# Performance work log

Measured on AMD Instinct MI355X. Metric: run time of the kernel, lower is better.

Reference implementation:

```python
import jax, jax.numpy as jnp
import numpy as np

B, T, I, U, S = 1024, 256, 64, 1024, 64  # batch, warmup_len, num_input_signals, units, output_steps


def setup_inputs() -> dict:
    key = jax.random.key(0)
    ks = jax.random.split(key, 4)
    s = lambda n: 1.0 / np.sqrt(n)
    inputs = jax.random.normal(ks[0], (B, T, I), jnp.float32)
    Wk = jax.random.normal(ks[1], (I, 4 * U), jnp.float32) * s(I)   # input kernel (gate order i,f,g,o)
    Wr = jax.random.normal(ks[2], (U, 4 * U), jnp.float32) * s(U)   # recurrent kernel
    b = jnp.zeros((4 * U,), jnp.float32)
    Wd = jax.random.normal(ks[3], (U, I), jnp.float32) * s(U)       # dense head
    bd = jnp.zeros((I,), jnp.float32)
    output_indices = jnp.arange(2, dtype=jnp.int32)
    return {"inputs": inputs, "Wk": Wk, "Wr": Wr, "b": b, "Wd": Wd, "bd": bd,
            "output_indices": output_indices, "output_steps": S}


def _lstm_step(h, c, x, Wk, Wr, b):
    # Keras LSTMCell math, gate order i, f, g(candidate), o
    z = x @ Wk + h @ Wr + b
    i, f, g, o = jnp.split(z, 4, axis=-1)
    c = jax.nn.sigmoid(f) * c + jax.nn.sigmoid(i) * jnp.tanh(g)
    h = jax.nn.sigmoid(o) * jnp.tanh(c)
    return h, c


def reference(inputs, Wk, Wr, b, Wd, bd, output_indices, output_steps):
    Bn = inputs.shape[0]
    Un = Wr.shape[0]
    h0 = jnp.zeros((Bn, Un), inputs.dtype)
    c0 = jnp.zeros((Bn, Un), inputs.dtype)

    # warmup: run LSTM over the input sequence, keep final state only
    def warm(carry, x_t):
        h, c = carry
        h, c = _lstm_step(h, c, x_t, Wk, Wr, b)
        return (h, c), None

    (h, c), _ = jax.lax.scan(warm, (h0, c0), jnp.swapaxes(inputs, 0, 1))
    pred = h @ Wd + bd  # first prediction [B, I]

    def dec(carry, _):
        h, c, p = carry
        h, c = _lstm_step(h, c, p, Wk, Wr, b)
        p = h @ Wd + bd
        return (h, c, p), p

    _, rest = jax.lax.scan(dec, (h, c, pred), None, length=output_steps - 1)
    preds = jnp.concatenate([pred[None], rest], axis=0)   # [S, B, I]
    preds = jnp.swapaxes(preds, 0, 1)                     # [B, S, I]
    return jnp.take(preds, output_indices, axis=-1)       # [B, S, len(output_indices)]
```

## Files before the change

### kernel.cpp

```cpp
#include <hip/hip_runtime.h>
#include <hip/hip_bf16.h>
#include <stdint.h>


typedef _Float16 f16;
typedef _Float16 f16x8 __attribute__((ext_vector_type(8)));
typedef float f32x4 __attribute__((ext_vector_type(4)));

#define TILE_HALVES 8192
#define NKZ 17
#define NKH 16

__device__ __forceinline__ int swz(int r, int k) { return (r * 64 + k) ^ ((r & 7) << 3); }

__device__ __forceinline__ void stage8k(const f16* __restrict__ g, f16* l, int tid) {
  const int wave = tid >> 6, lane = tid & 63;
  const char* gp = (const char*)g;
  char* lp = (char*)l;
#pragma unroll
  for (int i = 0; i < 4; i++) {
    const int off = i * 4096 + wave * 1024;
    __builtin_amdgcn_global_load_lds(
        (const __attribute__((address_space(1))) unsigned int*)(gp + off + lane * 16),
        (__attribute__((address_space(3))) unsigned int*)(lp + off), 16, 0, 0);
  }
}
__device__ __forceinline__ void stage4k(const f16* __restrict__ g, f16* l, int tid) {
  const int wave = tid >> 6, lane = tid & 63;
  const char* gp = (const char*)g;
  char* lp = (char*)l;
#pragma unroll
  for (int i = 0; i < 2; i++) {
    const int off = i * 4096 + wave * 1024;
    __builtin_amdgcn_global_load_lds(
        (const __attribute__((address_space(1))) unsigned int*)(gp + off + lane * 16),
        (__attribute__((address_space(3))) unsigned int*)(lp + off), 16, 0, 0);
  }
}

__device__ __forceinline__ float sigf(float x) { return 1.0f / (1.0f + __expf(-x)); }
__device__ __forceinline__ float tanhfast(float x) { return 1.0f - 2.0f / (__expf(2.0f * x) + 1.0f); }

__global__ void __launch_bounds__(256, 2) lstm_step(
    const f16* __restrict__ W16, const f16* __restrict__ Ax,
    const f16* __restrict__ hin, f16* __restrict__ hout,
    float* __restrict__ c32, const float* __restrict__ bperm) {
  const int tid = threadIdx.x;
  const int bid = blockIdx.x;
  const int xcd = bid & 7;
  const int ni = 4 * xcd + ((bid >> 3) & 3);
  const int mi = bid >> 5;

  __shared__ __align__(16) f16 As[2][4096];
  __shared__ __align__(16) f16 Bs[2][8192];

  f32x4 acc[2][4];
#pragma unroll
  for (int a = 0; a < 2; a++)
#pragma unroll
    for (int q = 0; q < 4; q++) acc[a][q] = (f32x4){0.f, 0.f, 0.f, 0.f};

  const f16* Ax0 = Ax + (size_t)(mi >> 1) * TILE_HALVES + (mi & 1) * 4096;
  const f16* Ah0 = hin + (size_t)(mi >> 1) * 16 * TILE_HALVES + (mi & 1) * 4096;
  const f16* Wb = W16 + (size_t)ni * NKZ * TILE_HALVES;

  stage4k(Ax0, As[0], tid);
  stage8k(Wb, Bs[0], tid);

  const int w = tid >> 6, lane = tid & 63;
  const int rw = w >> 1, cw = w & 1, ln15 = lane & 15, ln4 = lane >> 4;

  for (int kk = 0; kk < NKZ; kk++) {
    __syncthreads();
    if (kk + 1 < NKZ) {
      stage4k(Ah0 + (size_t)kk * TILE_HALVES, As[(kk + 1) & 1], tid);
      stage8k(Wb + (size_t)(kk + 1) * TILE_HALVES, Bs[(kk + 1) & 1], tid);
    }
    const f16* Ab = As[kk & 1];
    const f16* Bb = Bs[kk & 1];
#pragma unroll
    for (int kc = 0; kc < 2; kc++) {
      const int kb = kc * 32 + ln4 * 8;
      f16x8 af[2], bf[4];
#pragma unroll
      for (int mf = 0; mf < 2; mf++) {
        const int r = 32 * rw + 16 * mf + ln15;
        af[mf] = *(const f16x8*)(Ab + swz(r, kb));
      }
#pragma unroll
      for (int nf = 0; nf < 4; nf++) {
        const int n = 64 * cw + 16 * nf + ln15;
        bf[nf] = *(const f16x8*)(Bb + swz(n, kb));
      }
#pragma unroll
      for (int mf = 0; mf < 2; mf++)
#pragma unroll
        for (int nf = 0; nf < 4; nf++)
          acc[mf][nf] = __builtin_amdgcn_mfma_f32_16x16x32_f16(af[mf], bf[nf], acc[mf][nf], 0, 0, 0);
    }
  }

  const int u_glob = 32 * ni + 16 * cw + ln15;
  const int kkh = u_glob >> 6, kh = u_glob & 63;
  f16* ob = hout + ((size_t)(mi >> 1) * 16 + kkh) * TILE_HALVES;
  const float bi0 = bperm[ni * 128 + 64 * cw + 0 + ln15];
  const float bi1 = bperm[ni * 128 + 64 * cw + 16 + ln15];
  const float bi2 = bperm[ni * 128 + 64 * cw + 32 + ln15];
  const float bi3 = bperm[ni * 128 + 64 * cw + 48 + ln15];
#pragma unroll
  for (int mf = 0; mf < 2; mf++) {
#pragma unroll
    for (int reg = 0; reg < 4; reg++) {
      const int rl = 32 * rw + 16 * mf + 4 * ln4 + reg;
      const int brow = 64 * mi + rl;
      const int r128 = (mi & 1) * 64 + rl;
      const size_t cidx = (size_t)brow * 1024 + u_glob;
      const float zi = acc[mf][0][reg] + bi0;
      const float zf = acc[mf][1][reg] + bi1;
      const float zg = acc[mf][2][reg] + bi2;
      const float zo = acc[mf][3][reg] + bi3;
      const float co = c32[cidx];
      const float cn = sigf(zf) * co + sigf(zi) * tanhfast(zg);
      const float hn = sigf(zo) * tanhfast(cn);
      c32[cidx] = cn;
      ob[swz(r128, kh)] = (f16)hn;
    }
  }
}

__global__ void __launch_bounds__(256) head_kernel(
    const f16* __restrict__ Wd16, const f16* __restrict__ hin,
    f16* __restrict__ p16, const float* __restrict__ bd,
    const int* __restrict__ oidx, float* __restrict__ out,
    int n_idx, int s) {
  const int tid = threadIdx.x, mi = blockIdx.x;
  const int w = tid >> 6, lane = tid & 63, ln15 = lane & 15, ln4 = lane >> 4;

  __shared__ __align__(16) float red[3][16][292];

  f32x4 acc[4][4];
#pragma unroll
  for (int a = 0; a < 4; a++)
#pragma unroll
    for (int q = 0; q < 4; q++) acc[a][q] = (f32x4){0.f, 0.f, 0.f, 0.f};

  const size_t tile_base = (size_t)(mi >> 1) * 16;
  const int rhalf = (mi & 1) * 64;

#pragma unroll
  for (int kkl = 0; kkl < 4; kkl++) {
    const int kk_h = 4 * w + kkl;
    const f16* At = hin + (tile_base + kk_h) * TILE_HALVES;
    const f16* Bt = Wd16 + (size_t)kk_h * 4096;
#pragma unroll
    for (int kc = 0; kc < 2; kc++) {
      const int kb = kc * 32 + ln4 * 8;
      f16x8 af[4], bf[4];
#pragma unroll
      for (int mf = 0; mf < 4; mf++)
        af[mf] = *(const f16x8*)(At + swz(rhalf + 16 * mf + ln15, kb));
#pragma unroll
      for (int nf = 0; nf < 4; nf++)
        bf[nf] = *(const f16x8*)(Bt + swz(16 * nf + ln15, kb));
#pragma unroll
      for (int mf = 0; mf < 4; mf++)
#pragma unroll
        for (int nf = 0; nf < 4; nf++)
          acc[mf][nf] = __builtin_amdgcn_mfma_f32_16x16x32_f16(af[mf], bf[nf], acc[mf][nf], 0, 0, 0);
    }
  }

  const int lidx = lane * 4 + (lane >> 3) * 4;
  if (w > 0) {
#pragma unroll
    for (int mf = 0; mf < 4; mf++)
#pragma unroll
      for (int nf = 0; nf < 4; nf++)
        *(f32x4*)&red[w - 1][mf * 4 + nf][lidx] = acc[mf][nf];
  }
  __syncthreads();
  if (w == 0) {
#pragma unroll
    for (int mf = 0; mf < 4; mf++)
#pragma unroll
      for (int nf = 0; nf < 4; nf++) {
        const int slot = mf * 4 + nf;
        acc[mf][nf] += *(const f32x4*)&red[0][slot][lidx];
        acc[mf][nf] += *(const f32x4*)&red[1][slot][lidx];
        acc[mf][nf] += *(const f32x4*)&red[2][slot][lidx];
      }
#pragma unroll
    for (int mf = 0; mf < 4; mf++)
#pragma unroll
      for (int nf = 0; nf < 4; nf++) {
        const int col = 16 * nf + ln15;
        const float bdv = bd[col];
#pragma unroll
        for (int reg = 0; reg < 4; reg++) {
          const int rl = 16 * mf + 4 * ln4 + reg;
          const float pv = acc[mf][nf][reg] + bdv;
          p16[(size_t)(mi >> 1) * TILE_HALVES + swz(rhalf + rl, col)] = (f16)pv;
          const int brow = 64 * mi + rl;
          for (int oi = 0; oi < n_idx; oi++) {
            if (col == oidx[oi]) out[(size_t)brow * (64 * n_idx) + s * n_idx + oi] = pv;
          }
        }
      }
  }
}

__global__ void __launch_bounds__(256) prep_W(const float* __restrict__ Wk,
                                              const float* __restrict__ Wr,
                                              f16* __restrict__ W16) {
  const int blk = blockIdx.x;
  const int ni = blk / NKZ, kk = blk % NKZ;
  f16* ob = W16 + (size_t)blk * TILE_HALVES;
  for (int c = threadIdx.x; c < 1024; c += 256) {
    const int n = c >> 3, k0 = (c & 7) * 8;
    const int nf = n >> 4, j = n & 15;
    const int gate = nf & 3;
    const int u = 32 * ni + 16 * (nf >> 2) + j;
    const int col = gate * 1024 + u;
    f16x8 v;
#pragma unroll
    for (int e = 0; e < 8; e++) {
      const int kr = kk * 64 + k0 + e;
      const float val = (kr < 64) ? Wk[(size_t)kr * 4096 + col]
                                  : Wr[(size_t)(kr - 64) * 4096 + col];
      v[e] = (f16)val;
    }
    *(f16x8*)(ob + swz(n, k0)) = v;
  }
}

__global__ void __launch_bounds__(256) prep_Wd(const float* __restrict__ Wd, f16* __restrict__ Wd16) {
  const int kk = blockIdx.x;
  f16* ob = Wd16 + (size_t)kk * 4096;
  for (int c = threadIdx.x; c < 512; c += 256) {
    const int n = c >> 3, k0 = (c & 7) * 8;
    f16x8 v;
#pragma unroll
    for (int e = 0; e < 8; e++) {
      const int kr = kk * 64 + k0 + e;
      v[e] = (f16)Wd[(size_t)kr * 64 + n];
    }
    *(f16x8*)(ob + swz(n, k0)) = v;
  }
}

__global__ void __launch_bounds__(256) prep_X(const float* __restrict__ inp, f16* __restrict__ X16) {
  const int blk = blockIdx.x;
  const int t = blk >> 3, mi = blk & 7;
  f16* ob = X16 + (size_t)blk * TILE_HALVES;
  for (int c = threadIdx.x; c < 1024; c += 256) {
    const int r = c >> 3, k0 = (c & 7) * 8;
    const int b = 128 * mi + r;
    const float* src = inp + (size_t)b * 16384 + t * 64 + k0;
    const float4 x0 = *(const float4*)(src);
    const float4 x1 = *(const float4*)(src + 4);
    f16x8 v;
    v[0] = (f16)x0.x; v[1] = (f16)x0.y; v[2] = (f16)x0.z; v[3] = (f16)x0.w;
    v[4] = (f16)x1.x; v[5] = (f16)x1.y; v[6] = (f16)x1.z; v[7] = (f16)x1.w;
    *(f16x8*)(ob + swz(r, k0)) = v;
  }
}

__global__ void __launch_bounds__(256) prep_b(const float* __restrict__ b, float* __restrict__ bperm) {
  const int x = blockIdx.x * 256 + threadIdx.x;
  const int ni = x >> 7, rem = x & 127, nf = rem >> 4, j = rem & 15;
  bperm[x] = b[(nf & 3) * 1024 + 32 * ni + 16 * (nf >> 2) + j];
}

extern "C" void kernel_launch(void* const* d_in, const int* in_sizes, int n_in,
                              void* d_out, int out_size, void* d_ws, size_t ws_size,
                              hipStream_t stream) {
  const float* inputs = (const float*)d_in[0];
  const float* Wk = (const float*)d_in[1];
  const float* Wr = (const float*)d_in[2];
  const float* bv = (const float*)d_in[3];
  const float* Wd = (const float*)d_in[4];
  const float* bd = (const float*)d_in[5];
  const int* oidx = (const int*)d_in[6];
  float* out = (float*)d_out;
  const int n_idx = out_size / (1024 * 64);
  if (n_idx < 1) return;

  char* ws = (char*)d_ws;
  const size_t OFF_W16 = 0;
  const size_t OFF_WD16 = 8912896;
  const size_t OFF_BPERM = 9043968;
  const size_t OFF_C32 = 9060352;
  const size_t OFF_H0 = 13254656;
  const size_t OFF_H1 = 15351808;
  const size_t OFF_P16 = 17448960;
  const size_t OFF_X16 = 17580032;
  const size_t NEED = 51134464;
  if (ws_size < NEED) return;

  f16* W16 = (f16*)(ws + OFF_W16);
  f16* Wd16 = (f16*)(ws + OFF_WD16);
  float* bperm = (float*)(ws + OFF_BPERM);
  float* c32 = (float*)(ws + OFF_C32);
  f16* hb[2] = {(f16*)(ws + OFF_H0), (f16*)(ws + OFF_H1)};
  f16* p16 = (f16*)(ws + OFF_P16);
  f16* X16 = (f16*)(ws + OFF_X16);

  hipMemsetAsync(hb[0], 0, 2097152, stream);
  hipMemsetAsync(c32, 0, 4194304, stream);
  hipLaunchKernelGGL(prep_W, dim3(544), dim3(256), 0, stream, Wk, Wr, W16);
  hipLaunchKernelGGL(prep_Wd, dim3(16), dim3(256), 0, stream, Wd, Wd16);
  hipLaunchKernelGGL(prep_b, dim3(16), dim3(256), 0, stream, bv, bperm);
  hipLaunchKernelGGL(prep_X, dim3(2048), dim3(256), 0, stream, inputs, X16);

  for (int t = 0; t < 256; t++) {
    hipLaunchKernelGGL(lstm_step, dim3(512), dim3(256), 0, stream,
                       (const f16*)W16, (const f16*)(X16 + (size_t)t * 8 * TILE_HALVES),
                       (const f16*)hb[t & 1], hb[(t + 1) & 1], c32, (const float*)bperm);
  }
  for (int s = 0; s < 64; s++) {
    hipLaunchKernelGGL(head_kernel, dim3(16), dim3(256), 0, stream,
                       (const f16*)Wd16, (const f16*)hb[s & 1], p16, bd, oidx, out, n_idx, s);
    if (s < 63) {
      hipLaunchKernelGGL(lstm_step, dim3(512), dim3(256), 0, stream,
                         (const f16*)W16, (const f16*)p16,
                         (const f16*)hb[s & 1], hb[(s + 1) & 1], c32, (const float*)bperm);
    }
  }
}
```

Measured before the change: 6.901 ms.

## Fold dense head into recurrent weights and deepen LSTM step pipeline

Precomputes W' = Wr + Wd·Wk and b' = b + bd·Wk so decode steps run a 16-tile K loop on h alone, removing the separate head kernel and the p16 round-trip. Only the selected output columns are computed, via a per-thread dot product with a shuffle reduction and atomicAdd into an output buffer pre-initialised with bd. The step kernel moves to a triple-buffered LDS pipeline with explicit vmcnt waits and s_setprio around the MFMAs, and the cell state now uses a per-thread contiguous layout. The folded weights change fp16 rounding, and the atomics make output summation order nondeterministic.

```diff
diff --git a/kernel.cpp b/kernel.cpp
--- a/kernel.cpp
+++ b/kernel.cpp
@@ -9,7 +9,7 @@
 
 #define TILE_HALVES 8192
 #define NKZ 17
-#define NKH 16
+#define NKD 16
 
 __device__ __forceinline__ int swz(int r, int k) { return (r * 64 + k) ^ ((r & 7) << 3); }
 
@@ -42,42 +42,58 @@
 __device__ __forceinline__ float tanhfast(float x) { return 1.0f - 2.0f / (__expf(2.0f * x) + 1.0f); }
 
 __global__ void __launch_bounds__(256, 2) lstm_step(
-    const f16* __restrict__ W16, const f16* __restrict__ Ax,
+    const f16* __restrict__ Wp, const f16* __restrict__ Ax,
     const f16* __restrict__ hin, f16* __restrict__ hout,
-    float* __restrict__ c32, const float* __restrict__ bperm) {
+    float* __restrict__ c32p, const float* __restrict__ bperm,
+    const float* __restrict__ Wd, const int* __restrict__ oidx,
+    float* __restrict__ outp, int n_idx, int nkz) {
   const int tid = threadIdx.x;
   const int bid = blockIdx.x;
   const int xcd = bid & 7;
   const int ni = 4 * xcd + ((bid >> 3) & 3);
   const int mi = bid >> 5;
 
-  __shared__ __align__(16) f16 As[2][4096];
-  __shared__ __align__(16) f16 Bs[2][8192];
-
-  f32x4 acc[2][4];
-#pragma unroll
-  for (int a = 0; a < 2; a++)
-#pragma unroll
-    for (int q = 0; q < 4; q++) acc[a][q] = (f32x4){0.f, 0.f, 0.f, 0.f};
-
+  __shared__ __align__(16) f16 As[3][4096];
+  __shared__ __align__(16) f16 Bs[3][8192];
+
+  const int has_x = (Ax != nullptr) ? 1 : 0;
   const f16* Ax0 = Ax + (size_t)(mi >> 1) * TILE_HALVES + (mi & 1) * 4096;
   const f16* Ah0 = hin + (size_t)(mi >> 1) * 16 * TILE_HALVES + (mi & 1) * 4096;
-  const f16* Wb = W16 + (size_t)ni * NKZ * TILE_HALVES;
-
-  stage4k(Ax0, As[0], tid);
+  const f16* Wb = Wp + (size_t)ni * nkz * TILE_HALVES;
+
+  f32x4 acc[2][4];
+#pragma unroll
+  for (int a = 0; a < 2; a++)
+#pragma unroll
+    for (int q = 0; q < 4; q++) acc[a][q] = (f32x4){0.f, 0.f, 0.f, 0.f};
+
+  auto atile = [&](int kk) -> const f16* {
+    return (kk == 0 && has_x) ? Ax0 : (Ah0 + (size_t)(kk - has_x) * TILE_HALVES);
+  };
+
+  stage4k(atile(0), As[0], tid);
   stage8k(Wb, Bs[0], tid);
+  stage4k(atile(1), As[1], tid);
+  stage8k(Wb + TILE_HALVES, Bs[1], tid);
 
   const int w = tid >> 6, lane = tid & 63;
   const int rw = w >> 1, cw = w & 1, ln15 = lane & 15, ln4 = lane >> 4;
 
-  for (int kk = 0; kk < NKZ; kk++) {
-    __syncthreads();
-    if (kk + 1 < NKZ) {
-      stage4k(Ah0 + (size_t)kk * TILE_HALVES, As[(kk + 1) & 1], tid);
-      stage8k(Wb + (size_t)(kk + 1) * TILE_HALVES, Bs[(kk + 1) & 1], tid);
-    }
-    const f16* Ab = As[kk & 1];
-    const f16* Bb = Bs[kk & 1];
+  int cur = 0;
+  for (int kk = 0; kk < nkz; kk++) {
+    if (kk + 1 < nkz) {
+      asm volatile("s_waitcnt vmcnt(6)" ::: "memory");
+    } else {
+      asm volatile("s_waitcnt vmcnt(0)" ::: "memory");
+    }
+    __builtin_amdgcn_s_barrier();
+    if (kk + 2 < nkz) {
+      int wr = cur + 2; if (wr >= 3) wr -= 3;
+      stage4k(atile(kk + 2), As[wr], tid);
+      stage8k(Wb + (size_t)(kk + 2) * TILE_HALVES, Bs[wr], tid);
+    }
+    const f16* Ab = As[cur];
+    const f16* Bb = Bs[cur];
 #pragma unroll
     for (int kc = 0; kc < 2; kc++) {
       const int kb = kc * 32 + ln4 * 8;
@@ -92,12 +108,15 @@
         const int n = 64 * cw + 16 * nf + ln15;
         bf[nf] = *(const f16x8*)(Bb + swz(n, kb));
       }
+      __builtin_amdgcn_s_setprio(1);
 #pragma unroll
       for (int mf = 0; mf < 2; mf++)
 #pragma unroll
         for (int nf = 0; nf < 4; nf++)
           acc[mf][nf] = __builtin_amdgcn_mfma_f32_16x16x32_f16(af[mf], bf[nf], acc[mf][nf], 0, 0, 0);
-    }
+      __builtin_amdgcn_s_setprio(0);
+    }
+    cur = cur + 1; if (cur == 3) cur = 0;
   }
 
   const int u_glob = 32 * ni + 16 * cw + ln15;
@@ -107,105 +126,52 @@
   const float bi1 = bperm[ni * 128 + 64 * cw + 16 + ln15];
   const float bi2 = bperm[ni * 128 + 64 * cw + 32 + ln15];
   const float bi3 = bperm[ni * 128 + 64 * cw + 48 + ln15];
+
+  float* cp = c32p + ((size_t)bid * 256 + tid) * 8;
+  f32x4 cold0 = *(const f32x4*)(cp);
+  f32x4 cold1 = *(const f32x4*)(cp + 4);
+
+  float hv[2][4];
 #pragma unroll
   for (int mf = 0; mf < 2; mf++) {
+    f32x4 cn4;
 #pragma unroll
     for (int reg = 0; reg < 4; reg++) {
       const int rl = 32 * rw + 16 * mf + 4 * ln4 + reg;
-      const int brow = 64 * mi + rl;
       const int r128 = (mi & 1) * 64 + rl;
-      const size_t cidx = (size_t)brow * 1024 + u_glob;
       const float zi = acc[mf][0][reg] + bi0;
       const float zf = acc[mf][1][reg] + bi1;
       const float zg = acc[mf][2][reg] + bi2;
       const float zo = acc[mf][3][reg] + bi3;
-      const float co = c32[cidx];
+      const float co = (mf == 0) ? cold0[reg] : cold1[reg];
       const float cn = sigf(zf) * co + sigf(zi) * tanhfast(zg);
       const float hn = sigf(zo) * tanhfast(cn);
-      c32[cidx] = cn;
+      cn4[reg] = cn;
+      hv[mf][reg] = hn;
       ob[swz(r128, kh)] = (f16)hn;
     }
-  }
-}
-
-__global__ void __launch_bounds__(256) head_kernel(
-    const f16* __restrict__ Wd16, const f16* __restrict__ hin,
-    f16* __restrict__ p16, const float* __restrict__ bd,
-    const int* __restrict__ oidx, float* __restrict__ out,
-    int n_idx, int s) {
-  const int tid = threadIdx.x, mi = blockIdx.x;
-  const int w = tid >> 6, lane = tid & 63, ln15 = lane & 15, ln4 = lane >> 4;
-
-  __shared__ __align__(16) float red[3][16][292];
-
-  f32x4 acc[4][4];
-#pragma unroll
-  for (int a = 0; a < 4; a++)
-#pragma unroll
-    for (int q = 0; q < 4; q++) acc[a][q] = (f32x4){0.f, 0.f, 0.f, 0.f};
-
-  const size_t tile_base = (size_t)(mi >> 1) * 16;
-  const int rhalf = (mi & 1) * 64;
-
-#pragma unroll
-  for (int kkl = 0; kkl < 4; kkl++) {
-    const int kk_h = 4 * w + kkl;
-    const f16* At = hin + (tile_base + kk_h) * TILE_HALVES;
-    const f16* Bt = Wd16 + (size_t)kk_h * 4096;
-#pragma unroll
-    for (int kc = 0; kc < 2; kc++) {
-      const int kb = kc * 32 + ln4 * 8;
-      f16x8 af[4], bf[4];
-#pragma unroll
-      for (int mf = 0; mf < 4; mf++)
-        af[mf] = *(const f16x8*)(At + swz(rhalf + 16 * mf + ln15, kb));
-#pragma unroll
-      for (int nf = 0; nf < 4; nf++)
-        bf[nf] = *(const f16x8*)(Bt + swz(16 * nf + ln15, kb));
-#pragma unroll
-      for (int mf = 0; mf < 4; mf++)
-#pragma unroll
-        for (int nf = 0; nf < 4; nf++)
-          acc[mf][nf] = __builtin_amdgcn_mfma_f32_16x16x32_f16(af[mf], bf[nf], acc[mf][nf], 0, 0, 0);
-    }
-  }
-
-  const int lidx = lane * 4 + (lane >> 3) * 4;
-  if (w > 0) {
-#pragma unroll
-    for (int mf = 0; mf < 4; mf++)
-#pragma unroll
-      for (int nf = 0; nf < 4; nf++)
-        *(f32x4*)&red[w - 1][mf * 4 + nf][lidx] = acc[mf][nf];
-  }
-  __syncthreads();
-  if (w == 0) {
-#pragma unroll
-    for (int mf = 0; mf < 4; mf++)
-#pragma unroll
-      for (int nf = 0; nf < 4; nf++) {
-        const int slot = mf * 4 + nf;
-        acc[mf][nf] += *(const f32x4*)&red[0][slot][lidx];
-        acc[mf][nf] += *(const f32x4*)&red[1][slot][lidx];
-        acc[mf][nf] += *(const f32x4*)&red[2][slot][lidx];
-      }
-#pragma unroll
-    for (int mf = 0; mf < 4; mf++)
-#pragma unroll
-      for (int nf = 0; nf < 4; nf++) {
-        const int col = 16 * nf + ln15;
-        const float bdv = bd[col];
+    *(f32x4*)(cp + mf * 4) = cn4;
+  }
+
+  if (outp != nullptr) {
+    const int ostride = 64 * n_idx;
+    for (int j = 0; j < n_idx; j++) {
+      const float wdj = Wd[(size_t)u_glob * 64 + oidx[j]];
+#pragma unroll
+      for (int mf = 0; mf < 2; mf++)
 #pragma unroll
         for (int reg = 0; reg < 4; reg++) {
-          const int rl = 16 * mf + 4 * ln4 + reg;
-          const float pv = acc[mf][nf][reg] + bdv;
-          p16[(size_t)(mi >> 1) * TILE_HALVES + swz(rhalf + rl, col)] = (f16)pv;
-          const int brow = 64 * mi + rl;
-          for (int oi = 0; oi < n_idx; oi++) {
-            if (col == oidx[oi]) out[(size_t)brow * (64 * n_idx) + s * n_idx + oi] = pv;
+          float v = hv[mf][reg] * wdj;
+          v += __shfl_xor(v, 1);
+          v += __shfl_xor(v, 2);
+          v += __shfl_xor(v, 4);
+          v += __shfl_xor(v, 8);
+          if (ln15 == 0) {
+            const int brow = 64 * mi + 32 * rw + 16 * mf + 4 * ln4 + reg;
+            atomicAdd(&outp[(size_t)brow * ostride + j], v);
           }
         }
-      }
+    }
   }
 }
 
@@ -233,17 +199,33 @@
   }
 }
 
-__global__ void __launch_bounds__(256) prep_Wd(const float* __restrict__ Wd, f16* __restrict__ Wd16) {
-  const int kk = blockIdx.x;
-  f16* ob = Wd16 + (size_t)kk * 4096;
-  for (int c = threadIdx.x; c < 512; c += 256) {
+__global__ void __launch_bounds__(256) prep_Wp(const float* __restrict__ Wk,
+                                               const float* __restrict__ Wr,
+                                               const float* __restrict__ Wd,
+                                               f16* __restrict__ WP16) {
+  const int blk = blockIdx.x;
+  const int ni = blk / NKD, kk = blk % NKD;
+  f16* ob = WP16 + (size_t)blk * TILE_HALVES;
+  for (int c = threadIdx.x; c < 1024; c += 256) {
     const int n = c >> 3, k0 = (c & 7) * 8;
+    const int nf = n >> 4, j = n & 15;
+    const int gate = nf & 3;
+    const int u = 32 * ni + 16 * (nf >> 2) + j;
+    const int col = gate * 1024 + u;
+    const int uh0 = kk * 64 + k0;
+    float accv[8];
+#pragma unroll
+    for (int e = 0; e < 8; e++) accv[e] = Wr[(size_t)(uh0 + e) * 4096 + col];
+#pragma unroll
+    for (int i = 0; i < 64; i++) {
+      const float wki = Wk[(size_t)i * 4096 + col];
+#pragma unroll
+      for (int e = 0; e < 8; e++)
+        accv[e] += Wd[(size_t)(uh0 + e) * 64 + i] * wki;
+    }
     f16x8 v;
 #pragma unroll
-    for (int e = 0; e < 8; e++) {
-      const int kr = kk * 64 + k0 + e;
-      v[e] = (f16)Wd[(size_t)kr * 64 + n];
-    }
+    for (int e = 0; e < 8; e++) v[e] = (f16)accv[e];
     *(f16x8*)(ob + swz(n, k0)) = v;
   }
 }
@@ -271,6 +253,27 @@
   bperm[x] = b[(nf & 3) * 1024 + 32 * ni + 16 * (nf >> 2) + j];
 }
 
+__global__ void __launch_bounds__(256) prep_b2(const float* __restrict__ b,
+                                               const float* __restrict__ bd,
+                                               const float* __restrict__ Wk,
+                                               float* __restrict__ bperm2) {
+  const int x = blockIdx.x * 256 + threadIdx.x;
+  const int ni = x >> 7, rem = x & 127, nf = rem >> 4, j = rem & 15;
+  const int col = (nf & 3) * 1024 + 32 * ni + 16 * (nf >> 2) + j;
+  float acc = b[col];
+#pragma unroll
+  for (int i = 0; i < 64; i++) acc += bd[i] * Wk[(size_t)i * 4096 + col];
+  bperm2[x] = acc;
+}
+
+__global__ void __launch_bounds__(256) out_init(float* __restrict__ out,
+                                                const float* __restrict__ bd,
+                                                const int* __restrict__ oidx,
+                                                int n_idx, int total) {
+  const int x = blockIdx.x * 256 + threadIdx.x;
+  if (x < total) out[x] = bd[oidx[x % n_idx]];
+}
+
 extern "C" void kernel_launch(void* const* d_in, const int* in_sizes, int n_in,
                               void* d_out, int out_size, void* d_ws, size_t ws_size,
                               hipStream_t stream) {
@@ -287,43 +290,45 @@
 
   char* ws = (char*)d_ws;
   const size_t OFF_W16 = 0;
-  const size_t OFF_WD16 = 8912896;
-  const size_t OFF_BPERM = 9043968;
-  const size_t OFF_C32 = 9060352;
-  const size_t OFF_H0 = 13254656;
-  const size_t OFF_H1 = 15351808;
-  const size_t OFF_P16 = 17448960;
-  const size_t OFF_X16 = 17580032;
-  const size_t NEED = 51134464;
+  const size_t OFF_BPERM = 8912896;
+  const size_t OFF_C32 = 8929280;
+  const size_t OFF_H0 = 13123584;
+  const size_t OFF_H1 = 15220736;
+  const size_t OFF_X16 = 17317888;
+  const size_t NEED = 50872320;
   if (ws_size < NEED) return;
 
   f16* W16 = (f16*)(ws + OFF_W16);
-  f16* Wd16 = (f16*)(ws + OFF_WD16);
   float* bperm = (float*)(ws + OFF_BPERM);
-  float* c32 = (float*)(ws + OFF_C32);
+  float* c32p = (float*)(ws + OFF_C32);
   f16* hb[2] = {(f16*)(ws + OFF_H0), (f16*)(ws + OFF_H1)};
-  f16* p16 = (f16*)(ws + OFF_P16);
   f16* X16 = (f16*)(ws + OFF_X16);
+  f16* WP16 = (f16*)(ws + OFF_X16);
+  float* bperm2 = (float*)(ws + OFF_X16 + 8388608);
 
   hipMemsetAsync(hb[0], 0, 2097152, stream);
-  hipMemsetAsync(c32, 0, 4194304, stream);
+  hipMemsetAsync(c32p, 0, 4194304, stream);
   hipLaunchKernelGGL(prep_W, dim3(544), dim3(256), 0, stream, Wk, Wr, W16);
-  hipLaunchKernelGGL(prep_Wd, dim3(16), dim3(256), 0, stream, Wd, Wd16);
   hipLaunchKernelGGL(prep_b, dim3(16), dim3(256), 0, stream, bv, bperm);
   hipLaunchKernelGGL(prep_X, dim3(2048), dim3(256), 0, stream, inputs, X16);
-
-  for (int t = 0; t < 256; t++) {
+  {
+    const int total = 1024 * 64 * n_idx;
+    hipLaunchKernelGGL(out_init, dim3((total + 255) / 256), dim3(256), 0, stream,
+                       out, bd, oidx, n_idx, total);
+  }
+
+  for (int t = 0; t < 319; ++t) {
+    if (t == 256) {
+      hipLaunchKernelGGL(prep_Wp, dim3(512), dim3(256), 0, stream, Wk, Wr, Wd, WP16);
+      hipLaunchKernelGGL(prep_b2, dim3(16), dim3(256), 0, stream, bv, bd, Wk, bperm2);
+    }
+    const bool warm = (t < 256);
+    const f16* W = warm ? W16 : WP16;
+    const f16* Axp = warm ? (X16 + (size_t)t * 8 * TILE_HALVES) : nullptr;
+    const float* bp = warm ? bperm : bperm2;
+    float* op = (t >= 255) ? (out + (size_t)(t - 255) * n_idx) : nullptr;
     hipLaunchKernelGGL(lstm_step, dim3(512), dim3(256), 0, stream,
-                       (const f16*)W16, (const f16*)(X16 + (size_t)t * 8 * TILE_HALVES),
-                       (const f16*)hb[t & 1], hb[(t + 1) & 1], c32, (const float*)bperm);
-  }
-  for (int s = 0; s < 64; s++) {
-    hipLaunchKernelGGL(head_kernel, dim3(16), dim3(256), 0, stream,
-                       (const f16*)Wd16, (const f16*)hb[s & 1], p16, bd, oidx, out, n_idx, s);
-    if (s < 63) {
-      hipLaunchKernelGGL(lstm_step, dim3(512), dim3(256), 0, stream,
-                         (const f16*)W16, (const f16*)p16,
-                         (const f16*)hb[s & 1], hb[(s + 1) & 1], c32, (const float*)bperm);
-    }
-  }
-}
+                       W, Axp, (const f16*)hb[t & 1], hb[(t + 1) & 1],
+                       c32p, bp, Wd, oidx, op, n_idx, warm ? NKZ : NKD);
+  }
+}
```

After: 6.235 ms. 9.7% less time.
